# Kernel optimization log

Hardware: AMD Instinct MI355X
Metric: run time of the kernel (lower is better)

## Reference

```python
import jax, jax.numpy as jnp
import numpy as np

B, T, D, H = 8, 512, 1024, 16
DH = D // H  # per-head feature dim (64)


def setup_inputs() -> dict:
    key = jax.random.key(0)
    ks = jax.random.split(key, 10)
    s = 1.0 / np.sqrt(DH)
    inp = {
        "X_data": jax.random.normal(ks[0], (B, T, D), dtype=jnp.float32),
        "mask": jnp.ones((B, T), dtype=jnp.int32),
        # per-head Q/K/V projections (each SelfAttention has its own d_h x d_h weights)
        "Wq": jax.random.normal(ks[1], (H, DH, DH), dtype=jnp.float32) * s,
        "bq": jnp.zeros((H, DH), dtype=jnp.float32),
        "Wk": jax.random.normal(ks[2], (H, DH, DH), dtype=jnp.float32) * s,
        "bk": jnp.zeros((H, DH), dtype=jnp.float32),
        "Wv": jax.random.normal(ks[3], (H, DH, DH), dtype=jnp.float32) * s,
        "bv": jnp.zeros((H, DH), dtype=jnp.float32),
        # AttentionFusion: linear on concatenated head outputs -> len_feature_new
        "Wf": jax.random.normal(ks[4], (D, D), dtype=jnp.float32) * (1.0 / np.sqrt(D)),
        "bf": jnp.zeros((D,), dtype=jnp.float32),
    }
    return inp


def reference(X_data, mask, Wq, bq, Wk, bk, Wv, bv, Wf, bf):
    # Split features into heads: [B, T, H, DH] (equal partitions since D % H == 0)
    Xh = X_data.reshape(B, T, H, DH)
    # Batched per-head projections (replaces the Python loop over heads)
    Q = jnp.einsum("bthd,hde->bhte", Xh, Wq) + bq[None, :, None, :]
    K = jnp.einsum("bthd,hde->bhte", Xh, Wk) + bk[None, :, None, :]
    V = jnp.einsum("bthd,hde->bhte", Xh, Wv) + bv[None, :, None, :]
    scale = 1.0 / jnp.sqrt(jnp.asarray(DH, dtype=Q.dtype))
    scores = jnp.einsum("bhqe,bhke->bhqk", Q, K) * scale  # [B, H, T, T]
    scores = jnp.where(mask[:, None, None, :] > 0, scores, jnp.asarray(-1e9, scores.dtype))
    att = jax.nn.softmax(scores, axis=-1)
    out = jnp.einsum("bhqk,bhke->bhqe", att, V)  # [B, H, T, DH]
    # Concatenate heads (same order as the per-head loop) and fuse
    out = out.transpose(0, 2, 1, 3).reshape(B, T, D)
    fused = out @ Wf + bf  # AttentionFusion linear
    return fused
```

## Files before the change

### kernel.cpp

```cpp
#include <hip/hip_runtime.h>
#include <math.h>

#define B 8
#define T 512
#define D 1024
#define H 16
#define DH 64

typedef __bf16 bf16;
typedef __attribute__((ext_vector_type(8))) __bf16 bf16x8;
typedef __attribute__((ext_vector_type(4))) __bf16 bf16x4;
typedef __attribute__((ext_vector_type(4))) float f32x4;

__device__ __forceinline__ void gld16(const void* g, void* l) {
    __builtin_amdgcn_global_load_lds(
        (const __attribute__((address_space(1))) void*)g,
        (__attribute__((address_space(3))) void*)l, 16, 0, 0);
}


__global__ __launch_bounds__(256) void prep_kernel(
    const float* __restrict__ X,
    const float* __restrict__ Wq, const float* __restrict__ Wk,
    const float* __restrict__ Wv, const float* __restrict__ Wf,
    bf16* __restrict__ Xb, bf16* __restrict__ WqT, bf16* __restrict__ WkT,
    bf16* __restrict__ WvT, bf16* __restrict__ WfT)
{
    __shared__ bf16 Ts[64 * 72];
    const int blk = blockIdx.x, tid = threadIdx.x;
    if (blk < 256) {
        const float4* src = (const float4*)X + (size_t)blk * 4096;
        bf16x4* dst = (bf16x4*)Xb + (size_t)blk * 4096;
#pragma unroll
        for (int k = 0; k < 16; ++k) {
            const float4 v = src[k * 256 + tid];
            bf16x4 t;
            t[0] = (bf16)v.x; t[1] = (bf16)v.y; t[2] = (bf16)v.z; t[3] = (bf16)v.w;
            dst[k * 256 + tid] = t;
        }
    } else if (blk < 304) {
        const int idx = blk - 256, m = idx >> 4, h = idx & 15;
        const float* src = (m == 0 ? Wq : (m == 1 ? Wk : Wv)) + h * 4096;
        bf16* dst = (m == 0 ? WqT : (m == 1 ? WkT : WvT)) + h * 4096;
        for (int i = tid; i < 1024; i += 256) {
            const int d = i >> 4, eq = (i & 15) * 4;
            const float4 w = *(const float4*)(src + d * 64 + eq);
            Ts[(eq + 0) * 72 + d] = (bf16)w.x; Ts[(eq + 1) * 72 + d] = (bf16)w.y;
            Ts[(eq + 2) * 72 + d] = (bf16)w.z; Ts[(eq + 3) * 72 + d] = (bf16)w.w;
        }
        __syncthreads();
        for (int i = tid; i < 512; i += 256) {
            const int e = i >> 3, kc = (i & 7) * 8;
            *(bf16x8*)(dst + e * 64 + kc) = *(const bf16x8*)&Ts[e * 72 + kc];
        }
    } else {
        const int ti = blk - 304, k0 = (ti >> 4) * 64, n0 = (ti & 15) * 64;
        for (int i = tid; i < 1024; i += 256) {
            const int k = i >> 4, nq = (i & 15) * 4;
            const float4 w = *(const float4*)(Wf + (size_t)(k0 + k) * D + n0 + nq);
            Ts[(nq + 0) * 72 + k] = (bf16)w.x; Ts[(nq + 1) * 72 + k] = (bf16)w.y;
            Ts[(nq + 2) * 72 + k] = (bf16)w.z; Ts[(nq + 3) * 72 + k] = (bf16)w.w;
        }
        __syncthreads();
        for (int i = tid; i < 512; i += 256) {
            const int n = i >> 3, kc = (i & 7) * 8;
            *(bf16x8*)(WfT + (size_t)(n0 + n) * D + k0 + kc) = *(const bf16x8*)&Ts[n * 72 + kc];
        }
    }
}

__global__ __launch_bounds__(256) void qkv_mfma(
    const bf16* __restrict__ Xb,
    const bf16* __restrict__ WqT, const bf16* __restrict__ WkT,
    const bf16* __restrict__ WvT,
    const float* __restrict__ bq, const float* __restrict__ bk,
    const float* __restrict__ bv,
    bf16* __restrict__ Qb, bf16* __restrict__ Kb, bf16* __restrict__ Vtb)
{
    __shared__ bf16 Xs[128 * 64];
    __shared__ bf16 Wqs[64 * 64], Wks[64 * 64], Wvs[64 * 64];
    __shared__ bf16 Vt_l[64 * 136];

    const int bh = blockIdx.x >> 2, t0 = (blockIdx.x & 3) * 128;
    const int b = bh >> 4, h = bh & 15;
    const int tid = threadIdx.x, wave = tid >> 6, lane = tid & 63;
    const int quad = lane >> 4, l15 = lane & 15;
    const int lr = lane >> 3, lc = lane & 7;
    const int csw = (lc ^ lr) * 8;

    {
        const int r0 = wave * 32;
#pragma unroll
        for (int j = 0; j < 4; ++j)
            gld16(Xb + (size_t)(b * T + t0 + r0 + j * 8 + lr) * D + h * DH + csw,
                  &Xs[(r0 + j * 8) * 64]);
        const int r1 = wave * 16;
#pragma unroll
        for (int j = 0; j < 2; ++j) {
            gld16(WqT + (size_t)h * 4096 + (r1 + j * 8 + lr) * 64 + csw, &Wqs[(r1 + j * 8) * 64]);
            gld16(WkT + (size_t)h * 4096 + (r1 + j * 8 + lr) * 64 + csw, &Wks[(r1 + j * 8) * 64]);
            gld16(WvT + (size_t)h * 4096 + (r1 + j * 8 + lr) * 64 + csw, &Wvs[(r1 + j * 8) * 64]);
        }
    }
    __syncthreads();

    bf16x8 af[2][2];
#pragma unroll
    for (int mt = 0; mt < 2; ++mt)
#pragma unroll
        for (int ks = 0; ks < 2; ++ks) {
            const int row = wave * 32 + mt * 16 + l15;
            af[mt][ks] = *(const bf16x8*)&Xs[row * 64 + ((ks * 4 + quad) ^ (l15 & 7)) * 8];
        }

    auto compute = [&](const bf16* Bmat, f32x4 acc[2][4]) {
#pragma unroll
        for (int ks = 0; ks < 2; ++ks) {
            bf16x8 bfr[4];
#pragma unroll
            for (int nt = 0; nt < 4; ++nt)
                bfr[nt] = *(const bf16x8*)&Bmat[(nt * 16 + l15) * 64 + ((ks * 4 + quad) ^ (l15 & 7)) * 8];
#pragma unroll
            for (int mt = 0; mt < 2; ++mt)
#pragma unroll
                for (int nt = 0; nt < 4; ++nt)
                    acc[mt][nt] = __builtin_amdgcn_mfma_f32_16x16x32_bf16(
                        af[mt][ks], bfr[nt], acc[mt][nt], 0, 0, 0);
        }
    };

    const size_t bhTD = (size_t)bh * T * DH;

    {
        f32x4 acc[2][4] = {};
        compute(Wqs, acc);
#pragma unroll
        for (int mt = 0; mt < 2; ++mt)
#pragma unroll
            for (int nt = 0; nt < 4; ++nt) {
                const int e = nt * 16 + l15;
                const float bias = bq[h * DH + e];
#pragma unroll
                for (int reg = 0; reg < 4; ++reg) {
                    const int t = t0 + wave * 32 + mt * 16 + quad * 4 + reg;
                    Qb[bhTD + (size_t)t * DH + e] = (bf16)((acc[mt][nt][reg] + bias) * 0.125f);
                }
            }
    }
    {
        f32x4 acc[2][4] = {};
        compute(Wks, acc);
#pragma unroll
        for (int mt = 0; mt < 2; ++mt)
#pragma unroll
            for (int nt = 0; nt < 4; ++nt) {
                const int e = nt * 16 + l15;
                const float bias = bk[h * DH + e];
#pragma unroll
                for (int reg = 0; reg < 4; ++reg) {
                    const int t = t0 + wave * 32 + mt * 16 + quad * 4 + reg;
                    Kb[bhTD + (size_t)t * DH + e] = (bf16)(acc[mt][nt][reg] + bias);
                }
            }
    }
    {
        f32x4 acc[2][4] = {};
        compute(Wvs, acc);
#pragma unroll
        for (int mt = 0; mt < 2; ++mt)
#pragma unroll
            for (int nt = 0; nt < 4; ++nt) {
                const int e = nt * 16 + l15;
                const float bias = bv[h * DH + e];
#pragma unroll
                for (int reg = 0; reg < 4; ++reg) {
                    const int tl = wave * 32 + mt * 16 + quad * 4 + reg;
                    Vt_l[e * 136 + tl] = (bf16)(acc[mt][nt][reg] + bias);
                }
            }
    }
    __syncthreads();
    for (int i = tid; i < 1024; i += 256) {
        const int e = i >> 4, c = (i & 15) * 8;
        const bf16x8 t = *(const bf16x8*)&Vt_l[e * 136 + c];
        *(bf16x8*)(Vtb + (size_t)bh * DH * T + (size_t)e * T + t0 + c) = t;
    }
}

__global__ __launch_bounds__(256) void attn_mfma(
    const bf16* __restrict__ Qb, const bf16* __restrict__ Kb,
    const bf16* __restrict__ Vtb, const int* __restrict__ mask,
    bf16* __restrict__ Ob)
{
    __shared__ bf16 Ks[128 * 64];
    __shared__ bf16 Vts[64 * 128];
    __shared__ bf16 Pl[4][32 * 136];
    __shared__ int msk[128];

    const int bh = blockIdx.x >> 2, q0 = (blockIdx.x & 3) * 128;
    const int b = bh >> 4, h = bh & 15;
    const int tid = threadIdx.x, wave = tid >> 6, lane = tid & 63;
    const int quad = lane >> 4, l15 = lane & 15;
    const int lr = lane >> 3, lc = lane & 7;
    const int csw = (lc ^ lr) * 8;

    const size_t bhTD = (size_t)bh * T * DH;
    const size_t bhDT = (size_t)bh * DH * T;

    bf16x8 qf[2][2];
#pragma unroll
    for (int mt = 0; mt < 2; ++mt)
#pragma unroll
        for (int ks = 0; ks < 2; ++ks)
            qf[mt][ks] = *(const bf16x8*)(Qb + bhTD +
                (size_t)(q0 + wave * 32 + mt * 16 + l15) * DH + ks * 32 + quad * 8);

    f32x4 acc[2][4] = {};
    float lst[2][4] = {};

    for (int kt = 0; kt < 4; ++kt) {
        const int k0 = kt * 128;
        __syncthreads();
        {
            const int r0 = wave * 32;
#pragma unroll
            for (int j = 0; j < 4; ++j)
                gld16(Kb + bhTD + (size_t)(k0 + r0 + j * 8 + lr) * DH + csw,
                      &Ks[(r0 + j * 8) * 64]);
            const int e0 = wave * 16;
#pragma unroll
            for (int j = 0; j < 4; ++j) {
                const int er = j * 4 + (lane >> 4);
                const int csw2 = ((lane & 15) ^ er) * 8;
                gld16(Vtb + bhDT + (size_t)(e0 + er) * T + k0 + csw2,
                      &Vts[(e0 + j * 4) * 128]);
            }
            if (tid < 128) msk[tid] = mask[(size_t)b * T + k0 + tid];
        }
        __syncthreads();

#pragma unroll
        for (int nt = 0; nt < 8; ++nt) {
            const int krow = nt * 16 + l15;
            const bf16x8 kf0 = *(const bf16x8*)&Ks[krow * 64 + ((quad) ^ (l15 & 7)) * 8];
            const bf16x8 kf1 = *(const bf16x8*)&Ks[krow * 64 + ((4 + quad) ^ (l15 & 7)) * 8];
            const int mv = msk[krow];
#pragma unroll
            for (int mt = 0; mt < 2; ++mt) {
                f32x4 s = {};
                s = __builtin_amdgcn_mfma_f32_16x16x32_bf16(qf[mt][0], kf0, s, 0, 0, 0);
                s = __builtin_amdgcn_mfma_f32_16x16x32_bf16(qf[mt][1], kf1, s, 0, 0, 0);
#pragma unroll
                for (int reg = 0; reg < 4; ++reg) {
                    const float p = (mv > 0) ? __expf(s[reg]) : 0.f;
                    lst[mt][reg] += p;
                    Pl[wave][(mt * 16 + quad * 4 + reg) * 136 + nt * 16 + l15] = (bf16)p;
                }
            }
        }
        __builtin_amdgcn_wave_barrier();

#pragma unroll
        for (int kc = 0; kc < 4; ++kc) {
            const bf16x8 pf0 = *(const bf16x8*)&Pl[wave][(l15) * 136 + kc * 32 + quad * 8];
            const bf16x8 pf1 = *(const bf16x8*)&Pl[wave][(16 + l15) * 136 + kc * 32 + quad * 8];
#pragma unroll
            for (int nt = 0; nt < 4; ++nt) {
                const int erow = nt * 16 + l15;
                const bf16x8 vf = *(const bf16x8*)&Vts[erow * 128 + ((kc * 4 + quad) ^ (l15 & 15)) * 8];
                acc[0][nt] = __builtin_amdgcn_mfma_f32_16x16x32_bf16(pf0, vf, acc[0][nt], 0, 0, 0);
                acc[1][nt] = __builtin_amdgcn_mfma_f32_16x16x32_bf16(pf1, vf, acc[1][nt], 0, 0, 0);
            }
        }
    }

#pragma unroll
    for (int mt = 0; mt < 2; ++mt)
#pragma unroll
        for (int reg = 0; reg < 4; ++reg) {
            float l = lst[mt][reg];
            l += __shfl_xor(l, 1);
            l += __shfl_xor(l, 2);
            l += __shfl_xor(l, 4);
            l += __shfl_xor(l, 8);
            const float inv = 1.f / l;
            const int t = q0 + wave * 32 + mt * 16 + quad * 4 + reg;
#pragma unroll
            for (int nt = 0; nt < 4; ++nt)
                Ob[((size_t)b * T + t) * D + h * DH + nt * 16 + l15] =
                    (bf16)(acc[mt][nt][reg] * inv);
        }
}

__global__ __launch_bounds__(256) void fuse_mfma(
    const bf16* __restrict__ Ob, const bf16* __restrict__ WfT,
    const float* __restrict__ bfv, float* __restrict__ out)
{
    __shared__ bf16 As[128 * 64];
    __shared__ bf16 Bs[64 * 64];

    const int col0 = blockIdx.x * 64;
    const int row0 = blockIdx.y * 128;
    const int tid = threadIdx.x, wave = tid >> 6, lane = tid & 63;
    const int quad = lane >> 4, l15 = lane & 15;
    const int lr = lane >> 3, lc = lane & 7;
    const int csw = (lc ^ lr) * 8;
    const int wm = wave * 32;

    f32x4 acc[2][4] = {};

    for (int k0 = 0; k0 < D; k0 += 64) {
        __syncthreads();
#pragma unroll
        for (int j = 0; j < 4; ++j)
            gld16(Ob + (size_t)(row0 + wm + j * 8 + lr) * D + k0 + csw, &As[(wm + j * 8) * 64]);
#pragma unroll
        for (int j = 0; j < 2; ++j)
            gld16(WfT + (size_t)(col0 + wave * 16 + j * 8 + lr) * D + k0 + csw,
                  &Bs[(wave * 16 + j * 8) * 64]);
        __syncthreads();
#pragma unroll
        for (int ks = 0; ks < 2; ++ks) {
            bf16x8 af[2], bfr[4];
#pragma unroll
            for (int mt = 0; mt < 2; ++mt) {
                const int row = wm + mt * 16 + l15;
                af[mt] = *(const bf16x8*)&As[row * 64 + ((ks * 4 + quad) ^ (l15 & 7)) * 8];
            }
#pragma unroll
            for (int nt = 0; nt < 4; ++nt)
                bfr[nt] = *(const bf16x8*)&Bs[(nt * 16 + l15) * 64 + ((ks * 4 + quad) ^ (l15 & 7)) * 8];
#pragma unroll
            for (int mt = 0; mt < 2; ++mt)
#pragma unroll
                for (int nt = 0; nt < 4; ++nt)
                    acc[mt][nt] = __builtin_amdgcn_mfma_f32_16x16x32_bf16(af[mt], bfr[nt], acc[mt][nt], 0, 0, 0);
        }
    }

    float bias[4];
#pragma unroll
    for (int nt = 0; nt < 4; ++nt) bias[nt] = bfv[col0 + nt * 16 + l15];
#pragma unroll
    for (int mt = 0; mt < 2; ++mt)
#pragma unroll
        for (int reg = 0; reg < 4; ++reg) {
            const int r = row0 + wm + mt * 16 + quad * 4 + reg;
#pragma unroll
            for (int nt = 0; nt < 4; ++nt)
                out[(size_t)r * D + col0 + nt * 16 + l15] = acc[mt][nt][reg] + bias[nt];
        }
}

extern "C" void kernel_launch(void* const* d_in, const int* in_sizes, int n_in,
                              void* d_out, int out_size, void* d_ws, size_t ws_size,
                              hipStream_t stream) {
    const float* X   = (const float*)d_in[0];
    const int* mask  = (const int*)d_in[1];
    const float* Wq  = (const float*)d_in[2];
    const float* bq  = (const float*)d_in[3];
    const float* Wk  = (const float*)d_in[4];
    const float* bk  = (const float*)d_in[5];
    const float* Wv  = (const float*)d_in[6];
    const float* bv  = (const float*)d_in[7];
    const float* Wf  = (const float*)d_in[8];
    const float* bfv = (const float*)d_in[9];
    float* out = (float*)d_out;

    bf16* wsb = (bf16*)d_ws;
    const size_t QN = (size_t)B * H * T * DH;
    bf16* Qb  = wsb;
    bf16* Kb  = wsb + QN;
    bf16* Vtb = wsb + 2 * QN;
    bf16* Ob  = wsb + 3 * QN;
    bf16* WfT = wsb + 4 * QN;
    bf16* WqT = WfT + (size_t)D * D;
    bf16* WkT = WqT + H * DH * DH;
    bf16* WvT = WkT + H * DH * DH;
    bf16* Xb  = WvT + H * DH * DH;

    prep_kernel<<<dim3(560), 256, 0, stream>>>(X, Wq, Wk, Wv, Wf, Xb, WqT, WkT, WvT, WfT);
    qkv_mfma<<<dim3(B * H * 4), 256, 0, stream>>>(Xb, WqT, WkT, WvT, bq, bk, bv, Qb, Kb, Vtb);
    attn_mfma<<<dim3(B * H * 4), 256, 0, stream>>>(Qb, Kb, Vtb, mask, Ob);
    fuse_mfma<<<dim3(D / 64, (B * T) / 128), 256, 0, stream>>>(Ob, WfT, bfv, out);
}
```

Baseline: 133.6 us.

## Fuse X conversion into QKV, stage outputs through LDS, deepen fuse K tile

The fp32-to-bf16 conversion of X moves into the QKV kernel, which removes the separate Xb pass and its global round trip. Q, K, O and the final fp32 output are now staged through shared memory, so global stores are written as wide, coalesced vectors instead of scattered 2-byte or 4-byte stores. The fuse GEMM uses a K tile of 128 with a 16-way XOR swizzle, halving the number of barrier-separated loop iterations. Block indexing is reordered so that consecutive blocks cover different heads. The cost is more LDS use, extra barriers, and the loss of async global_load_lds for X.

```diff
diff --git a/kernel.cpp b/kernel.cpp
--- a/kernel.cpp
+++ b/kernel.cpp
@@ -19,27 +19,16 @@
 }
 
 
-__global__ __launch_bounds__(256) void prep_kernel(
-    const float* __restrict__ X,
+__global__ __launch_bounds__(256) void prep_w(
     const float* __restrict__ Wq, const float* __restrict__ Wk,
     const float* __restrict__ Wv, const float* __restrict__ Wf,
-    bf16* __restrict__ Xb, bf16* __restrict__ WqT, bf16* __restrict__ WkT,
+    bf16* __restrict__ WqT, bf16* __restrict__ WkT,
     bf16* __restrict__ WvT, bf16* __restrict__ WfT)
 {
     __shared__ bf16 Ts[64 * 72];
     const int blk = blockIdx.x, tid = threadIdx.x;
-    if (blk < 256) {
-        const float4* src = (const float4*)X + (size_t)blk * 4096;
-        bf16x4* dst = (bf16x4*)Xb + (size_t)blk * 4096;
-#pragma unroll
-        for (int k = 0; k < 16; ++k) {
-            const float4 v = src[k * 256 + tid];
-            bf16x4 t;
-            t[0] = (bf16)v.x; t[1] = (bf16)v.y; t[2] = (bf16)v.z; t[3] = (bf16)v.w;
-            dst[k * 256 + tid] = t;
-        }
-    } else if (blk < 304) {
-        const int idx = blk - 256, m = idx >> 4, h = idx & 15;
+    if (blk < 48) {
+        const int m = blk >> 4, h = blk & 15;
         const float* src = (m == 0 ? Wq : (m == 1 ? Wk : Wv)) + h * 4096;
         bf16* dst = (m == 0 ? WqT : (m == 1 ? WkT : WvT)) + h * 4096;
         for (int i = tid; i < 1024; i += 256) {
@@ -54,7 +43,7 @@
             *(bf16x8*)(dst + e * 64 + kc) = *(const bf16x8*)&Ts[e * 72 + kc];
         }
     } else {
-        const int ti = blk - 304, k0 = (ti >> 4) * 64, n0 = (ti & 15) * 64;
+        const int ti = blk - 48, k0 = (ti >> 4) * 64, n0 = (ti & 15) * 64;
         for (int i = tid; i < 1024; i += 256) {
             const int k = i >> 4, nq = (i & 15) * 4;
             const float4 w = *(const float4*)(Wf + (size_t)(k0 + k) * D + n0 + nq);
@@ -70,7 +59,7 @@
 }
 
 __global__ __launch_bounds__(256) void qkv_mfma(
-    const bf16* __restrict__ Xb,
+    const float* __restrict__ X,
     const bf16* __restrict__ WqT, const bf16* __restrict__ WkT,
     const bf16* __restrict__ WvT,
     const float* __restrict__ bq, const float* __restrict__ bk,
@@ -79,21 +68,26 @@
 {
     __shared__ bf16 Xs[128 * 64];
     __shared__ bf16 Wqs[64 * 64], Wks[64 * 64], Wvs[64 * 64];
-    __shared__ bf16 Vt_l[64 * 136];
-
-    const int bh = blockIdx.x >> 2, t0 = (blockIdx.x & 3) * 128;
+    __shared__ bf16 Stage[128 * 76];
+
+    const int bh = blockIdx.x & 127, t0 = (blockIdx.x >> 7) * 128;
     const int b = bh >> 4, h = bh & 15;
     const int tid = threadIdx.x, wave = tid >> 6, lane = tid & 63;
     const int quad = lane >> 4, l15 = lane & 15;
     const int lr = lane >> 3, lc = lane & 7;
     const int csw = (lc ^ lr) * 8;
 
+    for (int i = tid; i < 1024; i += 256) {
+        const int row = i >> 3, c = i & 7;
+        const float* src = X + (size_t)(b * T + t0 + row) * D + h * DH + c * 8;
+        const float4 x0 = *(const float4*)src;
+        const float4 x1 = *(const float4*)(src + 4);
+        bf16x8 t;
+        t[0] = (bf16)x0.x; t[1] = (bf16)x0.y; t[2] = (bf16)x0.z; t[3] = (bf16)x0.w;
+        t[4] = (bf16)x1.x; t[5] = (bf16)x1.y; t[6] = (bf16)x1.z; t[7] = (bf16)x1.w;
+        *(bf16x8*)&Xs[row * 64 + (c ^ (row & 7)) * 8] = t;
+    }
     {
-        const int r0 = wave * 32;
-#pragma unroll
-        for (int j = 0; j < 4; ++j)
-            gld16(Xb + (size_t)(b * T + t0 + r0 + j * 8 + lr) * D + h * DH + csw,
-                  &Xs[(r0 + j * 8) * 64]);
         const int r1 = wave * 16;
 #pragma unroll
         for (int j = 0; j < 2; ++j) {
@@ -138,14 +132,18 @@
         for (int mt = 0; mt < 2; ++mt)
 #pragma unroll
             for (int nt = 0; nt < 4; ++nt) {
-                const int e = nt * 16 + l15;
-                const float bias = bq[h * DH + e];
-#pragma unroll
-                for (int reg = 0; reg < 4; ++reg) {
-                    const int t = t0 + wave * 32 + mt * 16 + quad * 4 + reg;
-                    Qb[bhTD + (size_t)t * DH + e] = (bf16)((acc[mt][nt][reg] + bias) * 0.125f);
-                }
-            }
+                const float bias = bq[h * DH + nt * 16 + l15];
+#pragma unroll
+                for (int reg = 0; reg < 4; ++reg)
+                    Stage[(wave * 32 + mt * 16 + quad * 4 + reg) * 76 + nt * 16 + l15] =
+                        (bf16)((acc[mt][nt][reg] + bias) * 0.125f);
+            }
+        __syncthreads();
+        for (int i = tid; i < 1024; i += 256) {
+            const int row = i >> 3, c = (i & 7) * 8;
+            *(bf16x8*)(Qb + bhTD + (size_t)(t0 + row) * DH + c) = *(const bf16x8*)&Stage[row * 76 + c];
+        }
+        __syncthreads();
     }
     {
         f32x4 acc[2][4] = {};
@@ -154,14 +152,18 @@
         for (int mt = 0; mt < 2; ++mt)
 #pragma unroll
             for (int nt = 0; nt < 4; ++nt) {
-                const int e = nt * 16 + l15;
-                const float bias = bk[h * DH + e];
-#pragma unroll
-                for (int reg = 0; reg < 4; ++reg) {
-                    const int t = t0 + wave * 32 + mt * 16 + quad * 4 + reg;
-                    Kb[bhTD + (size_t)t * DH + e] = (bf16)(acc[mt][nt][reg] + bias);
-                }
-            }
+                const float bias = bk[h * DH + nt * 16 + l15];
+#pragma unroll
+                for (int reg = 0; reg < 4; ++reg)
+                    Stage[(wave * 32 + mt * 16 + quad * 4 + reg) * 76 + nt * 16 + l15] =
+                        (bf16)(acc[mt][nt][reg] + bias);
+            }
+        __syncthreads();
+        for (int i = tid; i < 1024; i += 256) {
+            const int row = i >> 3, c = (i & 7) * 8;
+            *(bf16x8*)(Kb + bhTD + (size_t)(t0 + row) * DH + c) = *(const bf16x8*)&Stage[row * 76 + c];
+        }
+        __syncthreads();
     }
     {
         f32x4 acc[2][4] = {};
@@ -175,15 +177,15 @@
 #pragma unroll
                 for (int reg = 0; reg < 4; ++reg) {
                     const int tl = wave * 32 + mt * 16 + quad * 4 + reg;
-                    Vt_l[e * 136 + tl] = (bf16)(acc[mt][nt][reg] + bias);
+                    Stage[e * 152 + tl] = (bf16)(acc[mt][nt][reg] + bias);
                 }
             }
-    }
-    __syncthreads();
-    for (int i = tid; i < 1024; i += 256) {
-        const int e = i >> 4, c = (i & 15) * 8;
-        const bf16x8 t = *(const bf16x8*)&Vt_l[e * 136 + c];
-        *(bf16x8*)(Vtb + (size_t)bh * DH * T + (size_t)e * T + t0 + c) = t;
+        __syncthreads();
+        for (int i = tid; i < 1024; i += 256) {
+            const int e = i >> 4, c = (i & 15) * 8;
+            *(bf16x8*)(Vtb + (size_t)bh * DH * T + (size_t)e * T + t0 + c) =
+                *(const bf16x8*)&Stage[e * 152 + c];
+        }
     }
 }
 
@@ -197,7 +199,7 @@
     __shared__ bf16 Pl[4][32 * 136];
     __shared__ int msk[128];
 
-    const int bh = blockIdx.x >> 2, q0 = (blockIdx.x & 3) * 128;
+    const int bh = blockIdx.x & 127, q0 = (blockIdx.x >> 7) * 128;
     const int b = bh >> 4, h = bh & 15;
     const int tid = threadIdx.x, wave = tid >> 6, lane = tid & 63;
     const int quad = lane >> 4, l15 = lane & 15;
@@ -274,6 +276,8 @@
         }
     }
 
+    __syncthreads();
+    bf16* Ostage = &Pl[0][0];
 #pragma unroll
     for (int mt = 0; mt < 2; ++mt)
 #pragma unroll
@@ -284,52 +288,62 @@
             l += __shfl_xor(l, 4);
             l += __shfl_xor(l, 8);
             const float inv = 1.f / l;
-            const int t = q0 + wave * 32 + mt * 16 + quad * 4 + reg;
+            const int row = wave * 32 + mt * 16 + quad * 4 + reg;
 #pragma unroll
             for (int nt = 0; nt < 4; ++nt)
-                Ob[((size_t)b * T + t) * D + h * DH + nt * 16 + l15] =
-                    (bf16)(acc[mt][nt][reg] * inv);
-        }
+                Ostage[row * 76 + nt * 16 + l15] = (bf16)(acc[mt][nt][reg] * inv);
+        }
+    __syncthreads();
+    for (int i = tid; i < 1024; i += 256) {
+        const int row = i >> 3, c = (i & 7) * 8;
+        *(bf16x8*)(Ob + ((size_t)b * T + q0 + row) * D + h * DH + c) =
+            *(const bf16x8*)&Ostage[row * 76 + c];
+    }
 }
 
 __global__ __launch_bounds__(256) void fuse_mfma(
     const bf16* __restrict__ Ob, const bf16* __restrict__ WfT,
     const float* __restrict__ bfv, float* __restrict__ out)
 {
-    __shared__ bf16 As[128 * 64];
-    __shared__ bf16 Bs[64 * 64];
+    __shared__ bf16 smem[128 * 128 + 64 * 128];
+    bf16* As = smem;
+    bf16* Bs = smem + 128 * 128;
 
     const int col0 = blockIdx.x * 64;
     const int row0 = blockIdx.y * 128;
     const int tid = threadIdx.x, wave = tid >> 6, lane = tid & 63;
     const int quad = lane >> 4, l15 = lane & 15;
-    const int lr = lane >> 3, lc = lane & 7;
-    const int csw = (lc ^ lr) * 8;
+    const int lr4 = lane >> 4, lc16 = lane & 15;
     const int wm = wave * 32;
 
     f32x4 acc[2][4] = {};
 
-    for (int k0 = 0; k0 < D; k0 += 64) {
-        __syncthreads();
-#pragma unroll
-        for (int j = 0; j < 4; ++j)
-            gld16(Ob + (size_t)(row0 + wm + j * 8 + lr) * D + k0 + csw, &As[(wm + j * 8) * 64]);
-#pragma unroll
-        for (int j = 0; j < 2; ++j)
-            gld16(WfT + (size_t)(col0 + wave * 16 + j * 8 + lr) * D + k0 + csw,
-                  &Bs[(wave * 16 + j * 8) * 64]);
-        __syncthreads();
-#pragma unroll
-        for (int ks = 0; ks < 2; ++ks) {
+    for (int k0 = 0; k0 < D; k0 += 128) {
+        __syncthreads();
+#pragma unroll
+        for (int j = 0; j < 8; ++j) {
+            const int row = wm + j * 4 + lr4;
+            gld16(Ob + (size_t)(row0 + row) * D + k0 + ((lc16 ^ (row & 15)) * 8),
+                  &As[(wm + j * 4) * 128]);
+        }
+#pragma unroll
+        for (int j = 0; j < 4; ++j) {
+            const int row = wave * 16 + j * 4 + lr4;
+            gld16(WfT + (size_t)(col0 + row) * D + k0 + ((lc16 ^ (row & 15)) * 8),
+                  &Bs[(wave * 16 + j * 4) * 128]);
+        }
+        __syncthreads();
+#pragma unroll
+        for (int ks = 0; ks < 4; ++ks) {
             bf16x8 af[2], bfr[4];
 #pragma unroll
             for (int mt = 0; mt < 2; ++mt) {
                 const int row = wm + mt * 16 + l15;
-                af[mt] = *(const bf16x8*)&As[row * 64 + ((ks * 4 + quad) ^ (l15 & 7)) * 8];
+                af[mt] = *(const bf16x8*)&As[row * 128 + ((ks * 4 + quad) ^ l15) * 8];
             }
 #pragma unroll
             for (int nt = 0; nt < 4; ++nt)
-                bfr[nt] = *(const bf16x8*)&Bs[(nt * 16 + l15) * 64 + ((ks * 4 + quad) ^ (l15 & 7)) * 8];
+                bfr[nt] = *(const bf16x8*)&Bs[(nt * 16 + l15) * 128 + ((ks * 4 + quad) ^ l15) * 8];
 #pragma unroll
             for (int mt = 0; mt < 2; ++mt)
 #pragma unroll
@@ -338,6 +352,8 @@
         }
     }
 
+    __syncthreads();
+    float* Ofs = (float*)smem;
     float bias[4];
 #pragma unroll
     for (int nt = 0; nt < 4; ++nt) bias[nt] = bfv[col0 + nt * 16 + l15];
@@ -345,11 +361,16 @@
     for (int mt = 0; mt < 2; ++mt)
 #pragma unroll
         for (int reg = 0; reg < 4; ++reg) {
-            const int r = row0 + wm + mt * 16 + quad * 4 + reg;
+            const int row = wm + mt * 16 + quad * 4 + reg;
 #pragma unroll
             for (int nt = 0; nt < 4; ++nt)
-                out[(size_t)r * D + col0 + nt * 16 + l15] = acc[mt][nt][reg] + bias[nt];
-        }
+                Ofs[row * 68 + nt * 16 + l15] = acc[mt][nt][reg] + bias[nt];
+        }
+    __syncthreads();
+    for (int i = tid; i < 2048; i += 256) {
+        const int row = i >> 4, c = (i & 15) * 4;
+        *(float4*)(out + (size_t)(row0 + row) * D + col0 + c) = *(const float4*)&Ofs[row * 68 + c];
+    }
 }
 
 extern "C" void kernel_launch(void* const* d_in, const int* in_sizes, int n_in,
@@ -377,10 +398,9 @@
     bf16* WqT = WfT + (size_t)D * D;
     bf16* WkT = WqT + H * DH * DH;
     bf16* WvT = WkT + H * DH * DH;
-    bf16* Xb  = WvT + H * DH * DH;
-
-    prep_kernel<<<dim3(560), 256, 0, stream>>>(X, Wq, Wk, Wv, Wf, Xb, WqT, WkT, WvT, WfT);
-    qkv_mfma<<<dim3(B * H * 4), 256, 0, stream>>>(Xb, WqT, WkT, WvT, bq, bk, bv, Qb, Kb, Vtb);
+
+    prep_w<<<dim3(304), 256, 0, stream>>>(Wq, Wk, Wv, Wf, WqT, WkT, WvT, WfT);
+    qkv_mfma<<<dim3(B * H * 4), 256, 0, stream>>>(X, WqT, WkT, WvT, bq, bk, bv, Qb, Kb, Vtb);
     attn_mfma<<<dim3(B * H * 4), 256, 0, stream>>>(Qb, Kb, Vtb, mask, Ob);
     fuse_mfma<<<dim3(D / 64, (B * T) / 128), 256, 0, stream>>>(Ob, WfT, bfv, out);
 }
```

After: 129.3 us. 3.2% less time.
